# Performance work log

Measured on AMD Instinct MI355X. Metric: run time of the kernel, lower is better.

The kernel has to match this reference:

```python
import jax, jax.numpy as jnp
import numpy as np

B, N, M = 4, 2048, 2048
D_IN = 1024
H, HS = 16, 64
D_OUT = 1024


def _xavier(key, shape):
    # xavier_uniform over last two dims (fan_in=shape[-2], fan_out=shape[-1])
    fan_in, fan_out = shape[-2], shape[-1]
    limit = float(np.sqrt(6.0 / (fan_in + fan_out)))
    return jax.random.uniform(key, shape, jnp.float32, -limit, limit)


def setup_inputs() -> dict:
    key = jax.random.key(0)
    ks = jax.random.split(key, 7)
    return {
        "query": jax.random.normal(ks[0], (B, N, D_IN), jnp.float32),
        "key": jax.random.normal(ks[1], (B, M, D_IN), jnp.float32),
        "value": jax.random.normal(ks[2], (B, M, D_IN), jnp.float32),
        "query_kernel": _xavier(ks[3], (H, D_IN, HS)),
        "key_kernel": _xavier(ks[4], (H, D_IN, HS)),
        "value_kernel": _xavier(ks[5], (H, D_IN, HS)),
        "projection_kernel": _xavier(ks[6], (H, HS, D_OUT)),
        "projection_bias": jnp.zeros((D_OUT,), jnp.float32),
    }


def reference(query, key, value, query_kernel, key_kernel, value_kernel,
              projection_kernel, projection_bias):
    # per-head projections: (B, N, H, HS)
    q = jnp.einsum('bni,hio->bnho', query, query_kernel)
    k = jnp.einsum('bmi,hio->bmho', key, key_kernel)
    v = jnp.einsum('bmi,hio->bmho', value, value_kernel)
    q = q / jnp.sqrt(jnp.asarray(HS, q.dtype))
    logits = jnp.einsum('bnho,bmho->bhnm', q, k)          # (B, H, N, M)
    attn = jax.nn.softmax(logits, axis=-1)
    mh = jnp.einsum('bhnm,bmhi->bnhi', attn, v)           # (B, N, H, HS)
    out = jnp.einsum('bnhi,hio->bno', mh, projection_kernel) + projection_bias
    return out
```

## Files before the change

kernel.cpp:

```cpp
#include <hip/hip_runtime.h>

typedef __attribute__((ext_vector_type(8))) __bf16 bf16x8;
typedef __attribute__((ext_vector_type(4))) float f32x4;
typedef __attribute__((ext_vector_type(16))) float f32x16;
typedef __attribute__((ext_vector_type(8))) unsigned short u16x8;

__device__ __forceinline__ unsigned short f2bf(float f) {
  unsigned int u = __builtin_bit_cast(unsigned int, f);
  u += 0x7FFFu + ((u >> 16) & 1u);
  return (unsigned short)(u >> 16);
}
__device__ __forceinline__ unsigned int cvtpk(float a, float b) {
  unsigned int r;
  asm("v_cvt_pk_bf16_f32 %0, %1, %2" : "=v"(r) : "v"(a), "v"(b));
  return r;
}

#define KDIM 1024

__global__ __launch_bounds__(256) void prep_all(const float* __restrict__ wq,
                                                const float* __restrict__ wk,
                                                const float* __restrict__ wv,
                                                const float* __restrict__ wp,
                                                unsigned short* __restrict__ Wq,
                                                unsigned short* __restrict__ Wk,
                                                unsigned short* __restrict__ Wv,
                                                unsigned short* __restrict__ Wp,
                                                const float* __restrict__ q,
                                                const float* __restrict__ k,
                                                const float* __restrict__ v,
                                                unsigned short* __restrict__ qb,
                                                unsigned short* __restrict__ kb,
                                                unsigned short* __restrict__ vb) {
  __shared__ float T[64][68];
  const int t = threadIdx.x;
  if (blockIdx.x >= 1024) {
    const int blk = blockIdx.x - 1024;
    const int s3 = blk >> 12;
    const int inner = blk & 4095;
    const float* in = s3 == 0 ? q : (s3 == 1 ? k : v);
    unsigned short* out = s3 == 0 ? qb : (s3 == 1 ? kb : vb);
    const long i = ((long)inner * 256 + t) * 8;
    float4 a = *reinterpret_cast<const float4*>(in + i);
    float4 b = *reinterpret_cast<const float4*>(in + i + 4);
    uint4 o;
    o.x = cvtpk(a.x, a.y);
    o.y = cvtpk(a.z, a.w);
    o.z = cvtpk(b.x, b.y);
    o.w = cvtpk(b.z, b.w);
    *reinterpret_cast<uint4*>(out + i) = o;
    return;
  }
  const int sel = blockIdx.x >> 8;
  const int blk = blockIdx.x & 255;
  const int r = t >> 2, c0 = (t & 3) * 16;
  if (sel < 3) {
    const float* w = sel == 0 ? wq : (sel == 1 ? wk : wv);
    unsigned short* out = sel == 0 ? Wq : (sel == 1 ? Wk : Wv);
    const float scale = sel == 0 ? 0.125f * 1.44269504089f : 1.0f;
    const int h = blk >> 4;
    const int k0 = (blk & 15) * 64;
    const float* src = w + h * 65536 + (k0 + r) * 64 + c0;
#pragma unroll
    for (int e = 0; e < 16; e += 4)
      *reinterpret_cast<float4*>(&T[r][c0 + e]) = *reinterpret_cast<const float4*>(src + e);
    __syncthreads();
    unsigned int pk[8];
#pragma unroll
    for (int e = 0; e < 8; ++e)
      pk[e] = cvtpk(T[c0 + 2 * e][r] * scale, T[c0 + 2 * e + 1][r] * scale);
    unsigned short* dst = out + (h * 64 + r) * 1024 + k0 + c0;
    *reinterpret_cast<uint4*>(dst) = *reinterpret_cast<uint4*>(pk);
    *reinterpret_cast<uint4*>(dst + 8) = *reinterpret_cast<uint4*>(pk + 4);
  } else {
    const int i0 = (blk >> 4) * 64;
    const int o0 = (blk & 15) * 64;
    const float* src = wp + (long)(i0 + r) * 1024 + o0 + c0;
#pragma unroll
    for (int e = 0; e < 16; e += 4)
      *reinterpret_cast<float4*>(&T[r][c0 + e]) = *reinterpret_cast<const float4*>(src + e);
    __syncthreads();
    unsigned int pk[8];
#pragma unroll
    for (int e = 0; e < 8; ++e)
      pk[e] = cvtpk(T[c0 + 2 * e][r], T[c0 + 2 * e + 1][r]);
    unsigned short* dst = Wp + (long)(o0 + r) * 1024 + i0 + c0;
    *reinterpret_cast<uint4*>(dst) = *reinterpret_cast<uint4*>(pk);
    *reinterpret_cast<uint4*>(dst + 8) = *reinterpret_cast<uint4*>(pk + 4);
  }
}

#define STAGE_B(buf, kk)                                                                   \
  _Pragma("unroll") for (int i = 0; i < 4; ++i) {                                          \
    const int seg = w * 4 + i;                                                             \
    const int row = seg * 8 + rowl;                                                        \
    const unsigned short* src =                                                            \
        Wt + (long)(bx * 128 + row) * KDIM + (kk) + ((chnk ^ (row & 7)) * 8);              \
    __builtin_amdgcn_global_load_lds((const __attribute__((address_space(1))) void*)src,   \
                                     (__attribute__((address_space(3))) void*)&Bs[(buf) * 8192 + seg * 512], \
                                     16, 0, 0);                                            \
  }
#define STAGE_A(buf, kk)                                                                   \
  _Pragma("unroll") for (int i = 0; i < 2; ++i) {                                          \
    const int seg = w * 2 + i;                                                             \
    const int row = seg * 8 + rowl;                                                        \
    const unsigned short* src =                                                            \
        Ap + ((long)by * 64 + row) * KDIM + (kk) + ((chnk ^ (row & 7)) * 8);               \
    __builtin_amdgcn_global_load_lds((const __attribute__((address_space(1))) void*)src,   \
                                     (__attribute__((address_space(3))) void*)&As[(buf) * 4096 + seg * 512], \
                                     16, 0, 0);                                            \
  }
#define GEMM_COMPUTE(buf)                                                                  \
  _Pragma("unroll") for (int kc = 0; kc < 2; ++kc) {                                       \
    const int chs = ((kc * 4 + lh) ^ (l15 & 7)) * 8;                                       \
    bf16x8 af[2], bfr[4];                                                                  \
    _Pragma("unroll") for (int mi = 0; mi < 2; ++mi)                                       \
        af[mi] = *reinterpret_cast<const bf16x8*>(&As[(buf) * 4096 + (wr + mi * 16 + l15) * 64 + chs]); \
    _Pragma("unroll") for (int ni = 0; ni < 4; ++ni)                                       \
        bfr[ni] = *reinterpret_cast<const bf16x8*>(&Bs[(buf) * 8192 + (wc + ni * 16 + l15) * 64 + chs]); \
    _Pragma("unroll") for (int mi = 0; mi < 2; ++mi)                                       \
      _Pragma("unroll") for (int ni = 0; ni < 4; ++ni)                                     \
          acc[mi][ni] = __builtin_amdgcn_mfma_f32_16x16x32_bf16(af[mi], bfr[ni], acc[mi][ni], 0, 0, 0); \
  }

__global__ __launch_bounds__(256) void gemm_qkv(const unsigned short* __restrict__ qa,
                                                const unsigned short* __restrict__ ka,
                                                const unsigned short* __restrict__ va,
                                                const unsigned short* __restrict__ Wq,
                                                const unsigned short* __restrict__ Wk,
                                                const unsigned short* __restrict__ Wv,
                                                unsigned short* __restrict__ qo,
                                                unsigned short* __restrict__ ko,
                                                unsigned short* __restrict__ vo) {
  __shared__ unsigned short As[2 * 64 * 64];
  __shared__ unsigned short Bs[2 * 128 * 64];
  const int f = blockIdx.x;
  const int xcd = f & 7;
  const int bx = (f >> 3) & 7;
  const int by8 = (f >> 6) & 15;
  const int z = f >> 10;
  const int by = by8 * 8 + xcd;
  const unsigned short* Ap = z == 0 ? qa : (z == 1 ? ka : va);
  const unsigned short* Wt = z == 0 ? Wq : (z == 1 ? Wk : Wv);
  unsigned short* Cp = z == 0 ? qo : (z == 1 ? ko : vo);
  const int t = threadIdx.x;
  const int lane = t & 63, w = t >> 6;
  const int wr = (w >> 1) * 32, wc = (w & 1) * 64;
  const int l15 = lane & 15, lh = lane >> 4;
  const int rowl = lane >> 3;
  const int chnk = lane & 7;

  f32x4 acc[2][4];
#pragma unroll
  for (int i = 0; i < 2; ++i)
#pragma unroll
    for (int j = 0; j < 4; ++j) acc[i][j] = {0.f, 0.f, 0.f, 0.f};

  STAGE_B(0, 0)
  STAGE_A(0, 0)
  __syncthreads();
  for (int k0 = 0; k0 < KDIM; k0 += 64) {
    const int cur = (k0 >> 6) & 1;
    if (k0 + 64 < KDIM) {
      STAGE_B(cur ^ 1, k0 + 64)
      STAGE_A(cur ^ 1, k0 + 64)
    }
    GEMM_COMPUTE(cur)
    __syncthreads();
  }

  const long rbase = (long)by * 64 + wr;
  const long cbase = (long)bx * 128 + wc;
#pragma unroll
  for (int ni = 0; ni < 4; ++ni) {
    const long col = cbase + ni * 16 + l15;
#pragma unroll
    for (int mi = 0; mi < 2; ++mi) {
      const long row = rbase + mi * 16 + lh * 4;
      if (z == 2) {
        uint2 val;
        val.x = cvtpk(acc[mi][ni][0], acc[mi][ni][1]);
        val.y = cvtpk(acc[mi][ni][2], acc[mi][ni][3]);
        *reinterpret_cast<uint2*>(
            &Cp[(row >> 11) * 2097152 + col * 2048 + (row & 2047)]) = val;
      } else {
#pragma unroll
        for (int j = 0; j < 4; ++j)
          Cp[(row + j) * KDIM + col] = f2bf(acc[mi][ni][j]);
      }
    }
  }
}

__global__ __launch_bounds__(256) void gemm_out(const unsigned short* __restrict__ Ap,
                                                const unsigned short* __restrict__ Wt,
                                                float* __restrict__ Cp,
                                                const float* __restrict__ bias) {
  __shared__ unsigned short As[2 * 64 * 64];
  __shared__ unsigned short Bs[2 * 128 * 64];
  const int f = blockIdx.x;
  const int xcd = f & 7;
  const int bx = (f >> 3) & 7;
  const int by = ((f >> 6) & 15) * 8 + xcd;
  const int t = threadIdx.x;
  const int lane = t & 63, w = t >> 6;
  const int wr = (w >> 1) * 32, wc = (w & 1) * 64;
  const int l15 = lane & 15, lh = lane >> 4;
  const int rowl = lane >> 3;
  const int chnk = lane & 7;

  f32x4 acc[2][4];
#pragma unroll
  for (int i = 0; i < 2; ++i)
#pragma unroll
    for (int j = 0; j < 4; ++j) acc[i][j] = {0.f, 0.f, 0.f, 0.f};

  STAGE_B(0, 0)
  STAGE_A(0, 0)
  __syncthreads();
  for (int k0 = 0; k0 < KDIM; k0 += 64) {
    const int cur = (k0 >> 6) & 1;
    if (k0 + 64 < KDIM) {
      STAGE_B(cur ^ 1, k0 + 64)
      STAGE_A(cur ^ 1, k0 + 64)
    }
    GEMM_COMPUTE(cur)
    __syncthreads();
  }

  const long rbase = (long)by * 64 + wr;
  const long cbase = (long)bx * 128 + wc;
#pragma unroll
  for (int ni = 0; ni < 4; ++ni) {
    const long col = cbase + ni * 16 + l15;
    const float bv = bias[col];
#pragma unroll
    for (int mi = 0; mi < 2; ++mi) {
      const long row = rbase + mi * 16 + lh * 4;
#pragma unroll
      for (int j = 0; j < 4; ++j)
        Cp[(row + j) * KDIM + col] = acc[mi][ni][j] + bv;
    }
  }
}

__global__ __launch_bounds__(256) void attn_k(const unsigned short* __restrict__ Qp,
                                              const unsigned short* __restrict__ Kp,
                                              const unsigned short* __restrict__ Vtg,
                                              unsigned short* __restrict__ Op) {
  constexpr int LST = 72;
  __shared__ unsigned short Kl[64 * LST];
  __shared__ unsigned short Vl[64 * LST];
  const int t = threadIdx.x;
  const int lane = t & 63, w = t >> 6;
  const int l31 = lane & 31;
  const int hi = lane >> 5;
  const int d = blockIdx.x;
  const int xcd = d & 7, ii = d >> 3;
  const int bh = xcd * 8 + (ii >> 4);
  const int qblk = ii & 15;
  const long base = (long)(bh >> 4) * 2097152 + (long)(bh & 15) * 64;
  const long vbase = (long)bh * 131072;
  const int n0 = qblk * 128;
  const int sr = t >> 2, sc = (t & 3) * 16;

  bf16x8 qb[4];
  {
    const unsigned short* qsrc = Qp + base + (long)(n0 + w * 32 + l31) * 1024 + hi * 8;
#pragma unroll
    for (int kc = 0; kc < 4; ++kc)
      qb[kc] = *reinterpret_cast<const bf16x8*>(qsrc + kc * 16);
  }

  const unsigned short* ksrc = Kp + base + (long)sr * 1024 + sc;
  const unsigned short* vsrc = Vtg + vbase + (long)sr * 2048 + sc;
  u16x8 kr0 = *reinterpret_cast<const u16x8*>(ksrc);
  u16x8 kr1 = *reinterpret_cast<const u16x8*>(ksrc + 8);
  u16x8 vr0 = *reinterpret_cast<const u16x8*>(vsrc);
  u16x8 vr1 = *reinterpret_cast<const u16x8*>(vsrc + 8);

  float lsum = 0.f;
  f32x16 accO0, accO1;
#pragma unroll
  for (int r = 0; r < 16; ++r) { accO0[r] = 0.f; accO1[r] = 0.f; }

  for (int m0 = 0; m0 < 2048; m0 += 64) {
    *reinterpret_cast<u16x8*>(&Kl[sr * LST + sc]) = kr0;
    *reinterpret_cast<u16x8*>(&Kl[sr * LST + sc + 8]) = kr1;
    *reinterpret_cast<u16x8*>(&Vl[sr * LST + sc]) = vr0;
    *reinterpret_cast<u16x8*>(&Vl[sr * LST + sc + 8]) = vr1;
    __syncthreads();
    if (m0 + 64 < 2048) {
      kr0 = *reinterpret_cast<const u16x8*>(ksrc + (long)(m0 + 64) * 1024);
      kr1 = *reinterpret_cast<const u16x8*>(ksrc + (long)(m0 + 64) * 1024 + 8);
      vr0 = *reinterpret_cast<const u16x8*>(vsrc + m0 + 64);
      vr1 = *reinterpret_cast<const u16x8*>(vsrc + m0 + 72);
    }

    f32x16 s0, s1;
#pragma unroll
    for (int r = 0; r < 16; ++r) { s0[r] = 0.f; s1[r] = 0.f; }
    __builtin_amdgcn_s_setprio(1);
#pragma unroll
    for (int kc = 0; kc < 4; ++kc) {
      bf16x8 ka0 = *reinterpret_cast<const bf16x8*>(&Kl[(l31) * LST + kc * 16 + hi * 8]);
      bf16x8 ka1 = *reinterpret_cast<const bf16x8*>(&Kl[(32 + l31) * LST + kc * 16 + hi * 8]);
      s0 = __builtin_amdgcn_mfma_f32_32x32x16_bf16(ka0, qb[kc], s0, 0, 0, 0);
      s1 = __builtin_amdgcn_mfma_f32_32x32x16_bf16(ka1, qb[kc], s1, 0, 0, 0);
    }
    __builtin_amdgcn_s_setprio(0);

    float lst = 0.f;
#pragma unroll
    for (int r = 0; r < 16; ++r) {
      s0[r] = __builtin_amdgcn_exp2f(s0[r]);
      s1[r] = __builtin_amdgcn_exp2f(s1[r]);
      lst += s0[r] + s1[r];
    }
    lsum += lst;

    unsigned int W0[8], W1[8];
#pragma unroll
    for (int j = 0; j < 8; ++j) {
      W0[j] = cvtpk(s0[2 * j], s0[2 * j + 1]);
      W1[j] = cvtpk(s1[2 * j], s1[2 * j + 1]);
    }

    __builtin_amdgcn_s_setprio(1);
#pragma unroll
    for (int kc4 = 0; kc4 < 4; ++kc4) {
      const unsigned int* Wm = (kc4 < 2) ? W0 : W1;
      const int b = 4 * (kc4 & 1);
      unsigned int sv1 = (unsigned int)__shfl_xor((int)(hi ? Wm[b] : Wm[b + 2]), 32);
      unsigned int sv2 = (unsigned int)__shfl_xor((int)(hi ? Wm[b + 1] : Wm[b + 3]), 32);
      union { unsigned int u[4]; bf16x8 v; } c;
      c.u[0] = hi ? sv1 : Wm[b];
      c.u[1] = hi ? sv2 : Wm[b + 1];
      c.u[2] = hi ? Wm[b + 2] : sv1;
      c.u[3] = hi ? Wm[b + 3] : sv2;
      bf16x8 vb0 = *reinterpret_cast<const bf16x8*>(&Vl[(l31) * LST + kc4 * 16 + hi * 8]);
      bf16x8 vb1 = *reinterpret_cast<const bf16x8*>(&Vl[(32 + l31) * LST + kc4 * 16 + hi * 8]);
      accO0 = __builtin_amdgcn_mfma_f32_32x32x16_bf16(c.v, vb0, accO0, 0, 0, 0);
      accO1 = __builtin_amdgcn_mfma_f32_32x32x16_bf16(c.v, vb1, accO1, 0, 0, 0);
    }
    __builtin_amdgcn_s_setprio(0);
    __syncthreads();
  }

  lsum += __shfl_xor(lsum, 32);
  float linv = 1.f / lsum;
#pragma unroll
  for (int r = 0; r < 16; ++r) {
    const int qrow = (r & 3) + 8 * (r >> 2) + 4 * hi;
    float lr = __shfl(linv, qrow);
    const long row = n0 + w * 32 + qrow;
    Op[base + row * 1024 + l31] = f2bf(accO0[r] * lr);
    Op[base + row * 1024 + 32 + l31] = f2bf(accO1[r] * lr);
  }
}

extern "C" void kernel_launch(void* const* d_in, const int* in_sizes, int n_in,
                              void* d_out, int out_size, void* d_ws, size_t ws_size,
                              hipStream_t stream) {
  const float* q    = (const float*)d_in[0];
  const float* k    = (const float*)d_in[1];
  const float* v    = (const float*)d_in[2];
  const float* wq   = (const float*)d_in[3];
  const float* wk   = (const float*)d_in[4];
  const float* wv   = (const float*)d_in[5];
  const float* wp   = (const float*)d_in[6];
  const float* bias = (const float*)d_in[7];

  unsigned short* ws = (unsigned short*)d_ws;
  unsigned short* Wq = ws;
  unsigned short* Wk = Wq + (1 << 20);
  unsigned short* Wv = Wk + (1 << 20);
  unsigned short* Wp = Wv + (1 << 20);
  unsigned short* qp = Wp + (1 << 20);
  unsigned short* kp = qp + (8 << 20);
  unsigned short* vt = kp + (8 << 20);
  unsigned short* mh = vt + (8 << 20);

  unsigned short* qb16 = (unsigned short*)d_out;
  unsigned short* kb16 = qb16 + (8 << 20);
  unsigned short* vb16 = mh;

  prep_all<<<13312, 256, 0, stream>>>(wq, wk, wv, wp, Wq, Wk, Wv, Wp,
                                      q, k, v, qb16, kb16, vb16);

  gemm_qkv<<<3072, 256, 0, stream>>>(qb16, kb16, vb16, Wq, Wk, Wv, qp, kp, vt);

  attn_k<<<1024, 256, 0, stream>>>(qp, kp, vt, mh);

  gemm_out<<<1024, 256, 0, stream>>>(mh, Wp, (float*)d_out, bias);
}
```

Baseline: 217.8 us.

## Double-buffer K/V tiles in LDS via direct global-to-LDS loads with XOR swizzle

```diff
diff --git a/kernel.cpp b/kernel.cpp
--- a/kernel.cpp
+++ b/kernel.cpp
@@ -248,9 +248,8 @@
                                               const unsigned short* __restrict__ Kp,
                                               const unsigned short* __restrict__ Vtg,
                                               unsigned short* __restrict__ Op) {
-  constexpr int LST = 72;
-  __shared__ unsigned short Kl[64 * LST];
-  __shared__ unsigned short Vl[64 * LST];
+  __shared__ unsigned short Kl[2 * 64 * 64];
+  __shared__ unsigned short Vl[2 * 64 * 64];
   const int t = threadIdx.x;
   const int lane = t & 63, w = t >> 6;
   const int l31 = lane & 31;
@@ -262,7 +261,8 @@
   const long base = (long)(bh >> 4) * 2097152 + (long)(bh & 15) * 64;
   const long vbase = (long)bh * 131072;
   const int n0 = qblk * 128;
-  const int sr = t >> 2, sc = (t & 3) * 16;
+  const int rowl = lane >> 3;
+  const int chnk = lane & 7;
 
   bf16x8 qb[4];
   {
@@ -272,30 +272,34 @@
       qb[kc] = *reinterpret_cast<const bf16x8*>(qsrc + kc * 16);
   }
 
-  const unsigned short* ksrc = Kp + base + (long)sr * 1024 + sc;
-  const unsigned short* vsrc = Vtg + vbase + (long)sr * 2048 + sc;
-  u16x8 kr0 = *reinterpret_cast<const u16x8*>(ksrc);
-  u16x8 kr1 = *reinterpret_cast<const u16x8*>(ksrc + 8);
-  u16x8 vr0 = *reinterpret_cast<const u16x8*>(vsrc);
-  u16x8 vr1 = *reinterpret_cast<const u16x8*>(vsrc + 8);
+#define STAGE_KV(buf, mm)                                                                  \
+  _Pragma("unroll") for (int i = 0; i < 2; ++i) {                                          \
+    const int seg = w * 2 + i;                                                             \
+    const int row = seg * 8 + rowl;                                                        \
+    const unsigned short* ksrc =                                                           \
+        Kp + base + (long)((mm) + row) * 1024 + ((chnk ^ rowl) * 8);                       \
+    __builtin_amdgcn_global_load_lds((const __attribute__((address_space(1))) void*)ksrc,  \
+                                     (__attribute__((address_space(3))) void*)&Kl[(buf) * 4096 + seg * 512], \
+                                     16, 0, 0);                                            \
+    const unsigned short* vsrc =                                                           \
+        Vtg + vbase + (long)row * 2048 + (mm) + ((chnk ^ rowl) * 8);                       \
+    __builtin_amdgcn_global_load_lds((const __attribute__((address_space(1))) void*)vsrc,  \
+                                     (__attribute__((address_space(3))) void*)&Vl[(buf) * 4096 + seg * 512], \
+                                     16, 0, 0);                                            \
+  }
 
   float lsum = 0.f;
   f32x16 accO0, accO1;
 #pragma unroll
   for (int r = 0; r < 16; ++r) { accO0[r] = 0.f; accO1[r] = 0.f; }
 
-  for (int m0 = 0; m0 < 2048; m0 += 64) {
-    *reinterpret_cast<u16x8*>(&Kl[sr * LST + sc]) = kr0;
-    *reinterpret_cast<u16x8*>(&Kl[sr * LST + sc + 8]) = kr1;
-    *reinterpret_cast<u16x8*>(&Vl[sr * LST + sc]) = vr0;
-    *reinterpret_cast<u16x8*>(&Vl[sr * LST + sc + 8]) = vr1;
-    __syncthreads();
-    if (m0 + 64 < 2048) {
-      kr0 = *reinterpret_cast<const u16x8*>(ksrc + (long)(m0 + 64) * 1024);
-      kr1 = *reinterpret_cast<const u16x8*>(ksrc + (long)(m0 + 64) * 1024 + 8);
-      vr0 = *reinterpret_cast<const u16x8*>(vsrc + m0 + 64);
-      vr1 = *reinterpret_cast<const u16x8*>(vsrc + m0 + 72);
-    }
+  STAGE_KV(0, 0)
+  __syncthreads();
+
+  const int sw = l31 & 7;
+  for (int tI = 0; tI < 32; ++tI) {
+    const int cur = tI & 1;
+    if (tI < 31) STAGE_KV(cur ^ 1, (tI + 1) * 64)
 
     f32x16 s0, s1;
 #pragma unroll
@@ -303,8 +307,9 @@
     __builtin_amdgcn_s_setprio(1);
 #pragma unroll
     for (int kc = 0; kc < 4; ++kc) {
-      bf16x8 ka0 = *reinterpret_cast<const bf16x8*>(&Kl[(l31) * LST + kc * 16 + hi * 8]);
-      bf16x8 ka1 = *reinterpret_cast<const bf16x8*>(&Kl[(32 + l31) * LST + kc * 16 + hi * 8]);
+      const int ch = (((kc << 1) + hi) ^ sw) * 8;
+      bf16x8 ka0 = *reinterpret_cast<const bf16x8*>(&Kl[cur * 4096 + l31 * 64 + ch]);
+      bf16x8 ka1 = *reinterpret_cast<const bf16x8*>(&Kl[cur * 4096 + (32 + l31) * 64 + ch]);
       s0 = __builtin_amdgcn_mfma_f32_32x32x16_bf16(ka0, qb[kc], s0, 0, 0, 0);
       s1 = __builtin_amdgcn_mfma_f32_32x32x16_bf16(ka1, qb[kc], s1, 0, 0, 0);
     }
@@ -338,8 +343,9 @@
       c.u[1] = hi ? sv2 : Wm[b + 1];
       c.u[2] = hi ? Wm[b + 2] : sv1;
       c.u[3] = hi ? Wm[b + 3] : sv2;
-      bf16x8 vb0 = *reinterpret_cast<const bf16x8*>(&Vl[(l31) * LST + kc4 * 16 + hi * 8]);
-      bf16x8 vb1 = *reinterpret_cast<const bf16x8*>(&Vl[(32 + l31) * LST + kc4 * 16 + hi * 8]);
+      const int ch = (((kc4 << 1) + hi) ^ sw) * 8;
+      bf16x8 vb0 = *reinterpret_cast<const bf16x8*>(&Vl[cur * 4096 + l31 * 64 + ch]);
+      bf16x8 vb1 = *reinterpret_cast<const bf16x8*>(&Vl[cur * 4096 + (32 + l31) * 64 + ch]);
       accO0 = __builtin_amdgcn_mfma_f32_32x32x16_bf16(c.v, vb0, accO0, 0, 0, 0);
       accO1 = __builtin_amdgcn_mfma_f32_32x32x16_bf16(c.v, vb1, accO1, 0, 0, 0);
     }
@@ -357,6 +363,7 @@
     Op[base + row * 1024 + l31] = f2bf(accO0[r] * lr);
     Op[base + row * 1024 + 32 + l31] = f2bf(accO1[r] * lr);
   }
+#undef STAGE_KV
 }
 
 extern "C" void kernel_launch(void* const* d_in, const int* in_sizes, int n_in,
```

Result: no change. 219.5 us (+0.8%).

## Double query rows per attention block to reuse K/V tiles

Applied to the files above, without the earlier changes.

```diff
diff --git a/kernel.cpp b/kernel.cpp
--- a/kernel.cpp
+++ b/kernel.cpp
@@ -244,10 +244,10 @@
   }
 }
 
-__global__ __launch_bounds__(256) void attn_k(const unsigned short* __restrict__ Qp,
-                                              const unsigned short* __restrict__ Kp,
-                                              const unsigned short* __restrict__ Vtg,
-                                              unsigned short* __restrict__ Op) {
+__global__ __launch_bounds__(256, 2) void attn_k(const unsigned short* __restrict__ Qp,
+                                                 const unsigned short* __restrict__ Kp,
+                                                 const unsigned short* __restrict__ Vtg,
+                                                 unsigned short* __restrict__ Op) {
   constexpr int LST = 72;
   __shared__ unsigned short Kl[64 * LST];
   __shared__ unsigned short Vl[64 * LST];
@@ -257,19 +257,22 @@
   const int hi = lane >> 5;
   const int d = blockIdx.x;
   const int xcd = d & 7, ii = d >> 3;
-  const int bh = xcd * 8 + (ii >> 4);
-  const int qblk = ii & 15;
+  const int bh = xcd * 8 + (ii >> 3);
+  const int qblk = ii & 7;
   const long base = (long)(bh >> 4) * 2097152 + (long)(bh & 15) * 64;
   const long vbase = (long)bh * 131072;
-  const int n0 = qblk * 128;
+  const int n0 = qblk * 256;
   const int sr = t >> 2, sc = (t & 3) * 16;
 
-  bf16x8 qb[4];
+  bf16x8 qbA[4], qbB[4];
   {
-    const unsigned short* qsrc = Qp + base + (long)(n0 + w * 32 + l31) * 1024 + hi * 8;
-#pragma unroll
-    for (int kc = 0; kc < 4; ++kc)
-      qb[kc] = *reinterpret_cast<const bf16x8*>(qsrc + kc * 16);
+    const unsigned short* qA = Qp + base + (long)(n0 + w * 64 + l31) * 1024 + hi * 8;
+    const unsigned short* qB = qA + 32 * 1024;
+#pragma unroll
+    for (int kc = 0; kc < 4; ++kc) {
+      qbA[kc] = *reinterpret_cast<const bf16x8*>(qA + kc * 16);
+      qbB[kc] = *reinterpret_cast<const bf16x8*>(qB + kc * 16);
+    }
   }
 
   const unsigned short* ksrc = Kp + base + (long)sr * 1024 + sc;
@@ -279,10 +282,10 @@
   u16x8 vr0 = *reinterpret_cast<const u16x8*>(vsrc);
   u16x8 vr1 = *reinterpret_cast<const u16x8*>(vsrc + 8);
 
-  float lsum = 0.f;
-  f32x16 accO0, accO1;
-#pragma unroll
-  for (int r = 0; r < 16; ++r) { accO0[r] = 0.f; accO1[r] = 0.f; }
+  float lsumA = 0.f, lsumB = 0.f;
+  f32x16 accA0, accA1, accB0, accB1;
+#pragma unroll
+  for (int r = 0; r < 16; ++r) { accA0[r] = 0.f; accA1[r] = 0.f; accB0[r] = 0.f; accB1[r] = 0.f; }
 
   for (int m0 = 0; m0 < 2048; m0 += 64) {
     *reinterpret_cast<u16x8*>(&Kl[sr * LST + sc]) = kr0;
@@ -297,65 +300,88 @@
       vr1 = *reinterpret_cast<const u16x8*>(vsrc + m0 + 72);
     }
 
-    f32x16 s0, s1;
-#pragma unroll
-    for (int r = 0; r < 16; ++r) { s0[r] = 0.f; s1[r] = 0.f; }
+    f32x16 sA0, sA1, sB0, sB1;
+#pragma unroll
+    for (int r = 0; r < 16; ++r) { sA0[r] = 0.f; sA1[r] = 0.f; sB0[r] = 0.f; sB1[r] = 0.f; }
     __builtin_amdgcn_s_setprio(1);
 #pragma unroll
     for (int kc = 0; kc < 4; ++kc) {
       bf16x8 ka0 = *reinterpret_cast<const bf16x8*>(&Kl[(l31) * LST + kc * 16 + hi * 8]);
       bf16x8 ka1 = *reinterpret_cast<const bf16x8*>(&Kl[(32 + l31) * LST + kc * 16 + hi * 8]);
-      s0 = __builtin_amdgcn_mfma_f32_32x32x16_bf16(ka0, qb[kc], s0, 0, 0, 0);
-      s1 = __builtin_amdgcn_mfma_f32_32x32x16_bf16(ka1, qb[kc], s1, 0, 0, 0);
+      sA0 = __builtin_amdgcn_mfma_f32_32x32x16_bf16(ka0, qbA[kc], sA0, 0, 0, 0);
+      sA1 = __builtin_amdgcn_mfma_f32_32x32x16_bf16(ka1, qbA[kc], sA1, 0, 0, 0);
+      sB0 = __builtin_amdgcn_mfma_f32_32x32x16_bf16(ka0, qbB[kc], sB0, 0, 0, 0);
+      sB1 = __builtin_amdgcn_mfma_f32_32x32x16_bf16(ka1, qbB[kc], sB1, 0, 0, 0);
     }
     __builtin_amdgcn_s_setprio(0);
 
-    float lst = 0.f;
+    float lstA = 0.f, lstB = 0.f;
 #pragma unroll
     for (int r = 0; r < 16; ++r) {
-      s0[r] = __builtin_amdgcn_exp2f(s0[r]);
-      s1[r] = __builtin_amdgcn_exp2f(s1[r]);
-      lst += s0[r] + s1[r];
-    }
-    lsum += lst;
-
-    unsigned int W0[8], W1[8];
+      sA0[r] = __builtin_amdgcn_exp2f(sA0[r]);
+      sA1[r] = __builtin_amdgcn_exp2f(sA1[r]);
+      lstA += sA0[r] + sA1[r];
+      sB0[r] = __builtin_amdgcn_exp2f(sB0[r]);
+      sB1[r] = __builtin_amdgcn_exp2f(sB1[r]);
+      lstB += sB0[r] + sB1[r];
+    }
+    lsumA += lstA;
+    lsumB += lstB;
+
+    unsigned int WA0[8], WA1[8], WB0[8], WB1[8];
 #pragma unroll
     for (int j = 0; j < 8; ++j) {
-      W0[j] = cvtpk(s0[2 * j], s0[2 * j + 1]);
-      W1[j] = cvtpk(s1[2 * j], s1[2 * j + 1]);
+      WA0[j] = cvtpk(sA0[2 * j], sA0[2 * j + 1]);
+      WA1[j] = cvtpk(sA1[2 * j], sA1[2 * j + 1]);
+      WB0[j] = cvtpk(sB0[2 * j], sB0[2 * j + 1]);
+      WB1[j] = cvtpk(sB1[2 * j], sB1[2 * j + 1]);
     }
 
     __builtin_amdgcn_s_setprio(1);
 #pragma unroll
     for (int kc4 = 0; kc4 < 4; ++kc4) {
-      const unsigned int* Wm = (kc4 < 2) ? W0 : W1;
+      const unsigned int* WmA = (kc4 < 2) ? WA0 : WA1;
+      const unsigned int* WmB = (kc4 < 2) ? WB0 : WB1;
       const int b = 4 * (kc4 & 1);
-      unsigned int sv1 = (unsigned int)__shfl_xor((int)(hi ? Wm[b] : Wm[b + 2]), 32);
-      unsigned int sv2 = (unsigned int)__shfl_xor((int)(hi ? Wm[b + 1] : Wm[b + 3]), 32);
-      union { unsigned int u[4]; bf16x8 v; } c;
-      c.u[0] = hi ? sv1 : Wm[b];
-      c.u[1] = hi ? sv2 : Wm[b + 1];
-      c.u[2] = hi ? Wm[b + 2] : sv1;
-      c.u[3] = hi ? Wm[b + 3] : sv2;
+      unsigned int a1 = (unsigned int)__shfl_xor((int)(hi ? WmA[b] : WmA[b + 2]), 32);
+      unsigned int a2 = (unsigned int)__shfl_xor((int)(hi ? WmA[b + 1] : WmA[b + 3]), 32);
+      unsigned int b1 = (unsigned int)__shfl_xor((int)(hi ? WmB[b] : WmB[b + 2]), 32);
+      unsigned int b2 = (unsigned int)__shfl_xor((int)(hi ? WmB[b + 1] : WmB[b + 3]), 32);
+      union { unsigned int u[4]; bf16x8 v; } cA, cB;
+      cA.u[0] = hi ? a1 : WmA[b];
+      cA.u[1] = hi ? a2 : WmA[b + 1];
+      cA.u[2] = hi ? WmA[b + 2] : a1;
+      cA.u[3] = hi ? WmA[b + 3] : a2;
+      cB.u[0] = hi ? b1 : WmB[b];
+      cB.u[1] = hi ? b2 : WmB[b + 1];
+      cB.u[2] = hi ? WmB[b + 2] : b1;
+      cB.u[3] = hi ? WmB[b + 3] : b2;
       bf16x8 vb0 = *reinterpret_cast<const bf16x8*>(&Vl[(l31) * LST + kc4 * 16 + hi * 8]);
       bf16x8 vb1 = *reinterpret_cast<const bf16x8*>(&Vl[(32 + l31) * LST + kc4 * 16 + hi * 8]);
-      accO0 = __builtin_amdgcn_mfma_f32_32x32x16_bf16(c.v, vb0, accO0, 0, 0, 0);
-      accO1 = __builtin_amdgcn_mfma_f32_32x32x16_bf16(c.v, vb1, accO1, 0, 0, 0);
+      accA0 = __builtin_amdgcn_mfma_f32_32x32x16_bf16(cA.v, vb0, accA0, 0, 0, 0);
+      accA1 = __builtin_amdgcn_mfma_f32_32x32x16_bf16(cA.v, vb1, accA1, 0, 0, 0);
+      accB0 = __builtin_amdgcn_mfma_f32_32x32x16_bf16(cB.v, vb0, accB0, 0, 0, 0);
+      accB1 = __builtin_amdgcn_mfma_f32_32x32x16_bf16(cB.v, vb1, accB1, 0, 0, 0);
     }
     __builtin_amdgcn_s_setprio(0);
     __syncthreads();
   }
 
-  lsum += __shfl_xor(lsum, 32);
-  float linv = 1.f / lsum;
+  lsumA += __shfl_xor(lsumA, 32);
+  lsumB += __shfl_xor(lsumB, 32);
+  float linvA = 1.f / lsumA;
+  float linvB = 1.f / lsumB;
 #pragma unroll
   for (int r = 0; r < 16; ++r) {
     const int qrow = (r & 3) + 8 * (r >> 2) + 4 * hi;
-    float lr = __shfl(linv, qrow);
-    const long row = n0 + w * 32 + qrow;
-    Op[base + row * 1024 + l31] = f2bf(accO0[r] * lr);
-    Op[base + row * 1024 + 32 + l31] = f2bf(accO1[r] * lr);
+    float lrA = __shfl(linvA, qrow);
+    float lrB = __shfl(linvB, qrow);
+    const long rowA = n0 + w * 64 + qrow;
+    const long rowB = rowA + 32;
+    Op[base + rowA * 1024 + l31] = f2bf(accA0[r] * lrA);
+    Op[base + rowA * 1024 + 32 + l31] = f2bf(accA1[r] * lrA);
+    Op[base + rowB * 1024 + l31] = f2bf(accB0[r] * lrB);
+    Op[base + rowB * 1024 + 32 + l31] = f2bf(accB1[r] * lrB);
   }
 }
 
@@ -390,7 +416,7 @@
 
   gemm_qkv<<<3072, 256, 0, stream>>>(qb16, kb16, vb16, Wq, Wk, Wv, qp, kp, vt);
 
-  attn_k<<<1024, 256, 0, stream>>>(qp, kp, vt, mh);
+  attn_k<<<512, 256, 0, stream>>>(qp, kp, vt, mh);
 
   gemm_out<<<1024, 256, 0, stream>>>(mh, Wp, (float*)d_out, bias);
 }
```

Measured after the change: 193.7 us. -11.1%, faster.
